# Kernel tuning notes

Measured on AMD Instinct MI355X. Metric: run time of the kernel, lower is better.

Reference implementation:

```python
import jax, jax.numpy as jnp
import numpy as np

# Mamba2 config (from init_kwargs + mamba_ssm Mamba2 defaults)
D_MODEL = 256
D_STATE = 16
D_CONV = 4
EXPAND = 2
HEADDIM = 64                      # Mamba2 default
D_INNER = EXPAND * D_MODEL        # 512
NHEADS = D_INNER // HEADDIM       # 8
CONV_DIM = D_INNER + 2 * D_STATE  # 544 (ngroups=1)
D_IN_PROJ = 2 * D_INNER + 2 * D_STATE + NHEADS  # 1064
B, H, W = 8, 64, 64
EPS = 1e-5


def setup_inputs() -> dict:
    key = jax.random.key(0)
    ks = jax.random.split(key, 8)
    x = jax.random.normal(ks[0], (B, D_MODEL, H, W), jnp.float32)
    ln_w = jnp.ones((D_MODEL,), jnp.float32)
    ln_b = jnp.zeros((D_MODEL,), jnp.float32)
    in_proj_w = jax.random.normal(ks[1], (D_IN_PROJ, D_MODEL), jnp.float32) * (D_MODEL ** -0.5)
    conv_w = jax.random.normal(ks[2], (CONV_DIM, D_CONV), jnp.float32) * (D_CONV ** -0.5)
    conv_b = jnp.zeros((CONV_DIM,), jnp.float32)
    dt = jax.random.uniform(ks[3], (NHEADS,), jnp.float32, 1e-3, 0.1)
    dt_bias = dt + jnp.log(-jnp.expm1(-dt))  # inverse softplus
    A_log = jnp.log(jax.random.uniform(ks[4], (NHEADS,), jnp.float32, 1.0, 16.0))
    D = jnp.ones((NHEADS,), jnp.float32)
    rms_w = jnp.ones((D_INNER,), jnp.float32)
    out_proj_w = jax.random.normal(ks[5], (D_MODEL, D_INNER), jnp.float32) * (D_INNER ** -0.5)
    return dict(x=x, ln_w=ln_w, ln_b=ln_b, in_proj_w=in_proj_w, conv_w=conv_w,
                conv_b=conv_b, dt_bias=dt_bias, A_log=A_log, D=D, rms_w=rms_w,
                out_proj_w=out_proj_w)


def reference(x, ln_w, ln_b, in_proj_w, conv_w, conv_b, dt_bias, A_log, D, rms_w, out_proj_w):
    Bb, C, Hh, Ww = x.shape
    L = Hh * Ww
    # (B,C,H,W) -> (B,L,C)
    xs = x.transpose(0, 2, 3, 1).reshape(Bb, L, C)
    # pre-LayerNorm
    mu = jnp.mean(xs, -1, keepdims=True)
    var = jnp.mean((xs - mu) ** 2, -1, keepdims=True)
    xn = (xs - mu) * jax.lax.rsqrt(var + EPS) * ln_w + ln_b
    # input projection -> z | xBC | dt
    zxbcdt = xn @ in_proj_w.T
    z = zxbcdt[..., :D_INNER]
    xBC = zxbcdt[..., D_INNER:D_INNER + CONV_DIM]
    dt = jax.nn.softplus(zxbcdt[..., D_INNER + CONV_DIM:] + dt_bias)  # (B,L,NH)
    # causal depthwise conv1d (kernel D_CONV) + SiLU
    xp = jnp.pad(xBC, ((0, 0), (D_CONV - 1, 0), (0, 0)))
    conv = conv_b
    for k in range(D_CONV):  # small fixed kernel loop
        conv = conv + xp[:, k:k + L, :] * conv_w[:, k]
    xBC = jax.nn.silu(conv)
    xh = xBC[..., :D_INNER].reshape(Bb, L, NHEADS, HEADDIM)
    Bm = xBC[..., D_INNER:D_INNER + D_STATE]   # (B,L,N)
    Cm = xBC[..., D_INNER + D_STATE:]          # (B,L,N)
    A = -jnp.exp(A_log)                        # (NH,)
    dA = jnp.exp(dt * A)                       # (B,L,NH)
    dtx = dt[..., None] * xh                   # (B,L,NH,P)

    def step(h, inp):
        dA_t, dtx_t, B_t, C_t = inp
        # h: (B,NH,P,N)
        h = dA_t[:, :, None, None] * h + dtx_t[..., None] * B_t[:, None, None, :]
        y = jnp.einsum('bhpn,bn->bhp', h, C_t)
        return h, y

    h0 = jnp.zeros((Bb, NHEADS, HEADDIM, D_STATE), xs.dtype)
    _, ys = jax.lax.scan(step, h0, (dA.transpose(1, 0, 2), dtx.transpose(1, 0, 2, 3),
                                    Bm.transpose(1, 0, 2), Cm.transpose(1, 0, 2)))
    y = ys.transpose(1, 0, 2, 3) + D[:, None] * xh   # (B,L,NH,P)
    y = y.reshape(Bb, L, D_INNER)
    # gated RMSNorm (norm_before_gate=False): rmsnorm(y * silu(z)) * w
    y = y * jax.nn.silu(z)
    y = y * jax.lax.rsqrt(jnp.mean(y * y, -1, keepdims=True) + EPS) * rms_w
    out = y @ out_proj_w.T
    out = out.reshape(Bb, Hh, Ww, C).transpose(0, 3, 1, 2) + x
    return out
```

## Files before the change

kernel.cpp:

```cpp
#include <hip/hip_runtime.h>
#include <cstdint>

typedef unsigned short u16;
typedef unsigned int u32;
typedef u16 u16x8 __attribute__((ext_vector_type(8)));
typedef u16 u16x4 __attribute__((ext_vector_type(4)));
typedef short short8 __attribute__((ext_vector_type(8)));
typedef float f32x4 __attribute__((ext_vector_type(4)));

__device__ __forceinline__ float bf2f(u16 u){ return __uint_as_float(((u32)u)<<16); }
__device__ __forceinline__ u16 f2bf(float f){
  u32 x = __float_as_uint(f);
  return (u16)((x + 0x7fffu + ((x>>16)&1u)) >> 16);
}
__device__ __forceinline__ float siluf(float v){ return v/(1.f + __expf(-v)); }


__global__ __launch_bounds__(256) void k0_wprep(const float* __restrict__ w1,
                                                const float* __restrict__ w2,
                                                u16* __restrict__ w1b, u16* __restrict__ w2b){
  u32 idx = blockIdx.x*256u + threadIdx.x;
  const u32 W1N = 1152u*256u;
  const u32 W2N = 256u*512u;
  if (idx < W1N){
    u32 n = idx >> 8;
    w1b[idx] = (n < 1064u) ? f2bf(w1[idx]) : (u16)0;
  } else if (idx < W1N + W2N){
    u32 j = idx - W1N;
    w2b[j] = f2bf(w2[j]);
  }
}

__global__ __launch_bounds__(256) void k1_ln(const float* __restrict__ x,
                                             const float* __restrict__ ln_w, const float* __restrict__ ln_b,
                                             const float* __restrict__ w1,
                                             u16* __restrict__ xnb, float* __restrict__ dtr){
  __shared__ float tile[256][33];
  __shared__ float mu_s[32], rs_s[32];
  const int b  = blockIdx.y;
  const int l0 = blockIdx.x*32;
  const int tid = threadIdx.x;
  const size_t xbase = (size_t)b*256*4096;
  const int cl = tid>>5;
  const int ll = tid&31;
  for (int cc=0; cc<256; cc+=8){
    int c = cc + cl;
    tile[c][ll] = x[xbase + (size_t)c*4096 + l0 + ll];
  }
  __syncthreads();
  const int lane = tid&63, wave = tid>>6;
  const int lidx = wave*8 + (lane&7);
  const int c0 = (lane>>3)*32;
  float s=0.f, ss=0.f;
  for (int c=c0; c<c0+32; ++c){ float v = tile[c][lidx]; s += v; ss += v*v; }
  for (int off=8; off<64; off<<=1){ s += __shfl_xor(s, off); ss += __shfl_xor(ss, off); }
  float mu = s*(1.f/256.f);
  float var = ss*(1.f/256.f) - mu*mu;
  float rs = rsqrtf(var + 1e-5f);
  if ((lane>>3)==0){ mu_s[lidx]=mu; rs_s[lidx]=rs; }
  __syncthreads();
  {
    const int c = tid;
    const float lw = ln_w[c], lb = ln_b[c];
    for (int l=0; l<32; ++l){
      float v = (tile[c][l]-mu_s[l])*rs_s[l]*lw + lb;
      xnb[((size_t)b*4096 + l0 + l)*256 + c] = f2bf(v);
    }
  }
  {
    const int r = tid>>3, j = tid&7;
    const float* wr = w1 + (size_t)(1056+j)*256;
    const float mur = mu_s[r], rsr = rs_s[r];
    float acc = 0.f;
    for (int c=0; c<256; ++c){
      float v = (tile[c][r]-mur)*rsr*ln_w[c] + ln_b[c];
      acc += v*wr[c];
    }
    dtr[((size_t)b*4096 + l0 + r)*8 + j] = acc;
  }
}

__global__ __launch_bounds__(256) void k2_gemm1(const u16* __restrict__ A, const u16* __restrict__ W,
                                                u16* __restrict__ zb, u16* __restrict__ xbcb){
  __shared__ u16 sA[128*40];
  __shared__ u16 sW[128*40];
  const int tid = threadIdx.x, lane = tid&63, wave = tid>>6;
  const size_t m0 = (size_t)blockIdx.y*128;
  const int n0 = blockIdx.x*128;
  const int wm = (wave>>1)*64, wn = (wave&1)*64;
  f32x4 acc[4][4] = {};
  const int fr = lane&15, kc = (lane>>4)*8;
  for (int k0=0; k0<256; k0+=32){
    #pragma unroll
    for (int j=0; j<2; ++j){
      int ch = j*256 + tid, r = ch>>2, co = (ch&3)*8;
      *(u16x8*)&sA[r*40+co] = *(const u16x8*)&A[(m0+r)*256 + k0 + co];
      *(u16x8*)&sW[r*40+co] = *(const u16x8*)&W[(size_t)(n0+r)*256 + k0 + co];
    }
    __syncthreads();
    short8 af[4], bf4[4];
    #pragma unroll
    for (int fm=0; fm<4; ++fm) af[fm]  = *(short8*)&sA[(wm+fm*16+fr)*40 + kc];
    #pragma unroll
    for (int fn=0; fn<4; ++fn) bf4[fn] = *(short8*)&sW[(wn+fn*16+fr)*40 + kc];
    #pragma unroll
    for (int fm=0; fm<4; ++fm)
      #pragma unroll
      for (int fn=0; fn<4; ++fn)
        acc[fm][fn] = __builtin_amdgcn_mfma_f32_16x16x32_bf16(af[fm],bf4[fn],acc[fm][fn],0,0,0);
    __syncthreads();
  }
  #pragma unroll
  for (int fm=0; fm<4; ++fm)
    #pragma unroll
    for (int fn=0; fn<4; ++fn){
      int rb = wm + fm*16 + ((lane>>4)<<2);
      int col = n0 + wn + fn*16 + (lane&15);
      #pragma unroll
      for (int i=0; i<4; ++i){
        size_t m = m0 + rb + i;
        float v = acc[fm][fn][i];
        if (col < 512)        zb[m*512 + col] = f2bf(v);
        else if (col < 1056)  xbcb[m*544 + (col-512)] = f2bf(v);
      }
    }
}

__global__ __launch_bounds__(256) void kU(const u16* __restrict__ xbcb, const float* __restrict__ dtr,
                                          const float* __restrict__ conv_w, const float* __restrict__ conv_b,
                                          const float* __restrict__ dt_bias, const float* __restrict__ A_log,
                                          float* __restrict__ hend, float* __restrict__ aprod){
  __shared__ char lds[44816];
  float* rawB = (float*)(lds + 0);
  u16*   BcT  = (u16*)(lds + 4560);
  float* wl   = (float*)(lds + 6864);
  const int ck = blockIdx.x, b = blockIdx.y, half = blockIdx.z;
  const int tid = threadIdx.x, lane = tid&63, hh = tid>>6;
  const int h = half*4 + hh;
  const int m0 = b*4096 + ck*64;
  u16* XW = (u16*)(lds + 7888 + hh*9232);
  for (int i=tid; i<67*16; i+=256){
    int r = i>>4, n = i&15; int l = ck*64 - 3 + r;
    rawB[r*17+n] = (l>=0) ? bf2f(xbcb[(size_t)(b*4096+l)*544 + 512 + n]) : 0.f;
  }
  {
    int t = lane;
    float dr = dtr[(size_t)(m0+t)*8 + h] + dt_bias[h];
    float dt = (dr > 20.f) ? dr : log1pf(__expf(dr));
    float Ah = -__expf(A_log[h]);
    float v = dt*Ah;
    #pragma unroll
    for (int off=1; off<64; off<<=1){ float p = __shfl_up(v, off); if (lane >= off) v += p; }
    float scT = __shfl(v, 63);
    wl[hh*64 + t] = dt * __expf(scT - v);
    if (lane==0) aprod[(b*8+h)*64 + ck] = __expf(scT);
  }
  __syncthreads();
  for (int i=tid; i<16*64; i+=256){
    int n = i>>6, s = i&63;
    int c = 512+n;
    float a = conv_b[c] + conv_w[c*4+0]*rawB[s*17+n] + conv_w[c*4+1]*rawB[(s+1)*17+n]
            + conv_w[c*4+2]*rawB[(s+2)*17+n] + conv_w[c*4+3]*rawB[(s+3)*17+n];
    BcT[n*72 + s] = f2bf(siluf(a));
  }
  {
    const int c = h*64 + lane;
    const float w0=conv_w[c*4], w1=conv_w[c*4+1], w2=conv_w[c*4+2], w3=conv_w[c*4+3];
    const float cb = conv_b[c];
    const int lb = ck*64;
    float xm3 = (lb>=3)? bf2f(xbcb[(size_t)(m0-3)*544 + c]) : 0.f;
    float xm2 = (lb>=2)? bf2f(xbcb[(size_t)(m0-2)*544 + c]) : 0.f;
    float xm1 = (lb>=1)? bf2f(xbcb[(size_t)(m0-1)*544 + c]) : 0.f;
    #pragma unroll 4
    for (int t=0; t<64; t+=2){
      float xc0 = bf2f(xbcb[(size_t)(m0+t)*544 + c]);
      float s0v = siluf(cb + w0*xm3 + w1*xm2 + w2*xm1 + w3*xc0) * wl[hh*64 + t];
      xm3=xm2; xm2=xm1; xm1=xc0;
      float xc1 = bf2f(xbcb[(size_t)(m0+t+1)*544 + c]);
      float s1v = siluf(cb + w0*xm3 + w1*xm2 + w2*xm1 + w3*xc1) * wl[hh*64 + t+1];
      xm3=xm2; xm2=xm1; xm1=xc1;
      *(u32*)&XW[lane*72 + t] = (u32)f2bf(s0v) | ((u32)f2bf(s1v)<<16);
    }
  }
  __syncthreads();
  const int fr = lane&15, g = lane>>4;
  f32x4 acc[4] = {};
  #pragma unroll
  for (int ks=0; ks<2; ++ks){
    short8 bfr = *(short8*)&BcT[fr*72 + ks*32 + g*8];
    #pragma unroll
    for (int ti=0; ti<4; ++ti){
      short8 afr = *(short8*)&XW[(ti*16+fr)*72 + ks*32 + g*8];
      acc[ti] = __builtin_amdgcn_mfma_f32_16x16x32_bf16(afr, bfr, acc[ti], 0,0,0);
    }
  }
  size_t hb = ((size_t)((b*8+h)*64 + ck))*64;
  #pragma unroll
  for (int ti=0; ti<4; ++ti)
    #pragma unroll
    for (int i=0; i<4; ++i){
      int p = ti*16 + g*4 + i;
      hend[(hb + p)*16 + fr] = acc[ti][i];
    }
}

__global__ __launch_bounds__(64) void k5_phase2(const float* __restrict__ hend, const float* __restrict__ aprod,
                                                float* __restrict__ hs){
  const int bh = blockIdx.x;
  const int lane = threadIdx.x;
  float hr[16];
  #pragma unroll
  for (int n=0;n<16;++n) hr[n]=0.f;
  for (int ck=0; ck<64; ++ck){
    size_t base = (((size_t)bh*64 + ck)*64 + lane)*16;
    float a = aprod[bh*64 + ck];
    #pragma unroll
    for (int n=0;n<16;++n) hs[base+n] = hr[n];
    #pragma unroll
    for (int n=0;n<16;++n) hr[n] = a*hr[n] + hend[base+n];
  }
}

__global__ __launch_bounds__(256) void kY(const u16* __restrict__ xbcb, const float* __restrict__ dtr,
                                          const float* __restrict__ conv_w, const float* __restrict__ conv_b,
                                          const float* __restrict__ dt_bias, const float* __restrict__ A_log,
                                          const float* __restrict__ Dp, const float* __restrict__ hs,
                                          u16* __restrict__ ybh){
  __shared__ char lds[58560];
  u16*   G     = (u16*)(lds + 0);
  float* rawBC = (float*)(lds + 0);
  u16*   Cc    = (u16*)(lds + 9216);
  u16*   Bc    = (u16*)(lds + 14336);
  float* scs   = (float*)(lds + 19456);
  float* dth   = (float*)(lds + 20544);
  const int ck = blockIdx.x, b = blockIdx.y, half = blockIdx.z;
  const int tid = threadIdx.x, lane = tid&63, hh = tid>>6;
  const int h = half*4 + hh;
  const int m0 = b*4096 + ck*64;
  u16* XT = (u16*)(lds + 21632 + hh*9232);
  for (int i=tid; i<67*32; i+=256){
    int r = i>>5, n = i&31; int l = ck*64 - 3 + r;
    rawBC[r*33+n] = (l>=0) ? bf2f(xbcb[(size_t)(b*4096+l)*544 + 512 + n]) : 0.f;
  }
  {
    int t = lane;
    float dr = dtr[(size_t)(m0+t)*8 + h] + dt_bias[h];
    float dt = (dr > 20.f) ? dr : log1pf(__expf(dr));
    float Ah = -__expf(A_log[h]);
    float v = dt*Ah;
    #pragma unroll
    for (int off=1; off<64; off<<=1){ float p = __shfl_up(v, off); if (lane >= off) v += p; }
    dth[hh*68 + t] = dt;
    scs[hh*68 + t] = v;
  }
  {
    const int c = h*64 + lane;
    const float w0=conv_w[c*4], w1=conv_w[c*4+1], w2=conv_w[c*4+2], w3=conv_w[c*4+3];
    const float cb = conv_b[c];
    const int lb = ck*64;
    float xm3 = (lb>=3)? bf2f(xbcb[(size_t)(m0-3)*544 + c]) : 0.f;
    float xm2 = (lb>=2)? bf2f(xbcb[(size_t)(m0-2)*544 + c]) : 0.f;
    float xm1 = (lb>=1)? bf2f(xbcb[(size_t)(m0-1)*544 + c]) : 0.f;
    #pragma unroll 4
    for (int t=0; t<64; t+=2){
      float xc0 = bf2f(xbcb[(size_t)(m0+t)*544 + c]);
      float s0v = siluf(cb + w0*xm3 + w1*xm2 + w2*xm1 + w3*xc0);
      xm3=xm2; xm2=xm1; xm1=xc0;
      float xc1 = bf2f(xbcb[(size_t)(m0+t+1)*544 + c]);
      float s1v = siluf(cb + w0*xm3 + w1*xm2 + w2*xm1 + w3*xc1);
      xm3=xm2; xm2=xm1; xm1=xc1;
      *(u32*)&XT[lane*72 + t] = (u32)f2bf(s0v) | ((u32)f2bf(s1v)<<16);
    }
  }
  __syncthreads();
  for (int i=tid; i<64*32; i+=256){
    int s = i>>5, n = i&31;
    int c = 512 + n;
    float a = conv_b[c] + conv_w[c*4+0]*rawBC[s*33+n] + conv_w[c*4+1]*rawBC[(s+1)*33+n]
            + conv_w[c*4+2]*rawBC[(s+2)*33+n] + conv_w[c*4+3]*rawBC[(s+3)*33+n];
    u16 v = f2bf(siluf(a));
    if (n < 16) Bc[s*40 + n] = v; else Cc[s*40 + (n-16)] = v;
  }
  for (int i=tid; i<64*16; i+=256){
    int s = i>>4, n = i&15;
    Bc[s*40 + 16 + n] = 0; Cc[s*40 + 16 + n] = 0;
  }
  __syncthreads();
  const int fr = lane&15, g = lane>>4;
  #define GFRAG(TI,SJ) { \
    short8 ca = *(short8*)&Cc[((TI)*16+fr)*40 + g*8]; \
    short8 bb = *(short8*)&Bc[((SJ)*16+fr)*40 + g*8]; \
    f32x4 d = {}; \
    d = __builtin_amdgcn_mfma_f32_16x16x32_bf16(ca, bb, d, 0,0,0); \
    G[((TI)*16 + g*4 + 0)*72 + (SJ)*16 + fr] = f2bf(d[0]); \
    G[((TI)*16 + g*4 + 1)*72 + (SJ)*16 + fr] = f2bf(d[1]); \
    G[((TI)*16 + g*4 + 2)*72 + (SJ)*16 + fr] = f2bf(d[2]); \
    G[((TI)*16 + g*4 + 3)*72 + (SJ)*16 + fr] = f2bf(d[3]); }
  if      (hh==0){ GFRAG(0,0) GFRAG(2,1) GFRAG(3,2) }
  else if (hh==1){ GFRAG(1,0) GFRAG(2,2) GFRAG(3,3) }
  else if (hh==2){ GFRAG(1,1) GFRAG(3,0) }
  else           { GFRAG(2,0) GFRAG(3,1) }
  #undef GFRAG
  __syncthreads();
  f32x4 acc[4][4] = {};
  {
    size_t hsbase = ((size_t)((b*8+h)*64 + ck))*64*16;
    short8 h0f[4];
    #pragma unroll
    for (int pj=0; pj<4; ++pj){
      short8 hf = {0,0,0,0,0,0,0,0};
      if (g < 2){
        int p = pj*16 + fr;
        f32x4 lo = *(const f32x4*)&hs[hsbase + p*16 + g*8];
        f32x4 hi = *(const f32x4*)&hs[hsbase + p*16 + g*8 + 4];
        #pragma unroll
        for (int kk=0; kk<4; ++kk){ hf[kk] = (short)f2bf(lo[kk]); hf[kk+4] = (short)f2bf(hi[kk]); }
      }
      h0f[pj] = hf;
    }
    #pragma unroll
    for (int ti=0; ti<4; ++ti){
      short8 ca = *(short8*)&Cc[(ti*16+fr)*40 + g*8];
      #pragma unroll
      for (int pj=0; pj<4; ++pj)
        acc[ti][pj] = __builtin_amdgcn_mfma_f32_16x16x32_bf16(ca, h0f[pj], acc[ti][pj], 0,0,0);
    }
  }
  #pragma unroll
  for (int ti=0; ti<4; ++ti)
    #pragma unroll
    for (int i=0; i<4; ++i){
      float pt = __expf(scs[hh*68 + ti*16 + g*4 + i]);
      #pragma unroll
      for (int pj=0; pj<4; ++pj) acc[ti][pj][i] *= pt;
    }
  #pragma unroll
  for (int ks=0; ks<2; ++ks){
    short8 xf[4];
    #pragma unroll
    for (int pj=0; pj<4; ++pj) xf[pj] = *(short8*)&XT[(pj*16+fr)*72 + ks*32 + g*8];
    #pragma unroll
    for (int ti=0; ti<4; ++ti){
      if (ks*32 > ti*16+15) continue;
      int t = ti*16 + fr;
      float sct = scs[hh*68 + t];
      f32x4 sc0 = *(f32x4*)&scs[hh*68 + ks*32 + g*8];
      f32x4 sc1 = *(f32x4*)&scs[hh*68 + ks*32 + g*8 + 4];
      f32x4 dt0 = *(f32x4*)&dth[hh*68 + ks*32 + g*8];
      f32x4 dt1 = *(f32x4*)&dth[hh*68 + ks*32 + g*8 + 4];
      u16x8 g8 = *(u16x8*)&G[t*72 + ks*32 + g*8];
      short8 mf;
      #pragma unroll
      for (int kk=0; kk<8; ++kk){
        int s = ks*32 + g*8 + kk;
        float sv = (kk<4) ? sc0[kk] : sc1[kk-4];
        float dv = (kk<4) ? dt0[kk] : dt1[kk-4];
        float m = (s <= t) ? bf2f(g8[kk]) * __expf(sct - sv) * dv : 0.f;
        mf[kk] = (short)f2bf(m);
      }
      #pragma unroll
      for (int pj=0; pj<4; ++pj)
        acc[ti][pj] = __builtin_amdgcn_mfma_f32_16x16x32_bf16(mf, xf[pj], acc[ti][pj], 0,0,0);
    }
  }
  {
    const float Dh = Dp[h];
    #pragma unroll
    for (int ti=0; ti<4; ++ti)
      #pragma unroll
      for (int pj=0; pj<4; ++pj){
        int p = pj*16 + fr;
        u16x4 xv = *(u16x4*)&XT[p*72 + ti*16 + g*4];
        #pragma unroll
        for (int i=0; i<4; ++i) acc[ti][pj][i] += Dh * bf2f(xv[i]);
      }
  }
  #pragma unroll
  for (int ti=0; ti<4; ++ti)
    #pragma unroll
    for (int pj=0; pj<4; ++pj)
      #pragma unroll
      for (int i=0; i<4; ++i)
        XT[(ti*16 + g*4 + i)*72 + pj*16 + fr] = f2bf(acc[ti][pj][i]);
  __syncthreads();
  {
    const int hl = lane>>4;
    const u16* R = (const u16*)(lds + 21632 + hl*9232);
    #pragma unroll
    for (int tt=0; tt<16; ++tt){
      int t = hh*16 + tt;
      u16x4 v = *(const u16x4*)&R[t*72 + (lane&15)*4];
      *(u16x4*)&ybh[(size_t)(m0+t)*512 + half*256 + lane*4] = v;
    }
  }
}

__global__ __launch_bounds__(256) void k7_rms(const u16* __restrict__ y, const u16* __restrict__ zb,
                                              const float* __restrict__ rms_w, u16* __restrict__ ynb){
  const int m = blockIdx.x*4 + (threadIdx.x>>6);
  const int lane = threadIdx.x&63;
  const size_t base = (size_t)m*512 + lane*8;
  u16x8 yv = *(const u16x8*)&y[base];
  u16x8 zv = *(const u16x8*)&zb[base];
  float g[8];
  float ssum = 0.f;
  #pragma unroll
  for (int j=0;j<8;++j){
    float zf = bf2f(zv[j]);
    float sig = 1.f/(1.f + __expf(-zf));
    g[j] = bf2f(yv[j]) * (zf*sig);
    ssum += g[j]*g[j];
  }
  for (int off=1; off<64; off<<=1) ssum += __shfl_xor(ssum, off);
  float rs = rsqrtf(ssum*(1.f/512.f) + 1e-5f);
  u16x8 o;
  #pragma unroll
  for (int j=0;j<8;++j) o[j] = f2bf(g[j]*rs*rms_w[lane*8+j]);
  *(u16x8*)&ynb[base] = o;
}

__global__ __launch_bounds__(256) void k8_gemm2(const u16* __restrict__ A, const u16* __restrict__ W,
                                                const float* __restrict__ xres, float* __restrict__ out){
  __shared__ float smem[4*64*65];
  u16* sA = (u16*)smem;
  u16* sW = ((u16*)smem) + 128*40;
  const int tid = threadIdx.x, lane = tid&63, wave = tid>>6;
  const size_t m0 = (size_t)blockIdx.y*128;
  const int n0 = blockIdx.x*128;
  const int wm = (wave>>1)*64, wn = (wave&1)*64;
  f32x4 acc[4][4] = {};
  const int fr = lane&15, kc = (lane>>4)*8;
  for (int k0=0; k0<512; k0+=32){
    #pragma unroll
    for (int j=0; j<2; ++j){
      int ch = j*256 + tid, r = ch>>2, co = (ch&3)*8;
      *(u16x8*)&sA[r*40+co] = *(const u16x8*)&A[(m0+r)*512 + k0 + co];
      *(u16x8*)&sW[r*40+co] = *(const u16x8*)&W[(size_t)(n0+r)*512 + k0 + co];
    }
    __syncthreads();
    short8 af[4], bf4[4];
    #pragma unroll
    for (int fm=0; fm<4; ++fm) af[fm]  = *(short8*)&sA[(wm+fm*16+fr)*40 + kc];
    #pragma unroll
    for (int fn=0; fn<4; ++fn) bf4[fn] = *(short8*)&sW[(wn+fn*16+fr)*40 + kc];
    #pragma unroll
    for (int fm=0; fm<4; ++fm)
      #pragma unroll
      for (int fn=0; fn<4; ++fn)
        acc[fm][fn] = __builtin_amdgcn_mfma_f32_16x16x32_bf16(af[fm],bf4[fn],acc[fm][fn],0,0,0);
    __syncthreads();
  }
  float* T = smem + wave*(64*65);
  #pragma unroll
  for (int fm=0; fm<4; ++fm)
    #pragma unroll
    for (int fn=0; fn<4; ++fn){
      int rr = fm*16 + ((lane>>4)<<2);
      int cc = fn*16 + (lane&15);
      #pragma unroll
      for (int i=0; i<4; ++i) T[(rr+i)*65 + cc] = acc[fm][fn][i];
    }
  __syncthreads();
  const int bb = (int)(m0>>12);
  const int lbase = (int)(m0&4095) + wm;
  for (int cc=0; cc<64; ++cc){
    int col = n0 + wn + cc;
    size_t o = ((size_t)bb*256 + col)*4096 + lbase + lane;
    out[o] = T[lane*65 + cc] + xres[o];
  }
}

extern "C" void kernel_launch(void* const* d_in, const int* in_sizes, int n_in,
                              void* d_out, int out_size, void* d_ws, size_t ws_size,
                              hipStream_t stream){
  const float* x        = (const float*)d_in[0];
  const float* ln_w     = (const float*)d_in[1];
  const float* ln_b     = (const float*)d_in[2];
  const float* in_proj  = (const float*)d_in[3];
  const float* conv_w   = (const float*)d_in[4];
  const float* conv_b   = (const float*)d_in[5];
  const float* dt_bias  = (const float*)d_in[6];
  const float* A_log    = (const float*)d_in[7];
  const float* Dp       = (const float*)d_in[8];
  const float* rms_w    = (const float*)d_in[9];
  const float* out_proj = (const float*)d_in[10];
  float* out = (float*)d_out;

  char* ws = (char*)d_ws;
  const size_t o_w1   = 0;
  const size_t o_w2   = 589824;
  const size_t o_xn   = 851968;
  const size_t o_z    = 17629184;
  const size_t o_xbcb = 51183616;
  const size_t o_dtr  = 86835200;
  const size_t o_hend = 87883776;
  const size_t o_hs   = 104660992;
  const size_t o_ap   = 121438208;
  const size_t o_ybh  = 121454592;
  const size_t NEED   = 155009024;
  if (ws_size < NEED) return;

  u16*   w1b  = (u16*)(ws + o_w1);
  u16*   w2b  = (u16*)(ws + o_w2);
  u16*   xnb  = (u16*)(ws + o_xn);
  u16*   zbuf = (u16*)(ws + o_z);
  u16*   xbcb = (u16*)(ws + o_xbcb);
  float* dtr  = (float*)(ws + o_dtr);
  float* hend = (float*)(ws + o_hend);
  float* hsb  = (float*)(ws + o_hs);
  float* ap   = (float*)(ws + o_ap);
  u16*   ybh  = (u16*)(ws + o_ybh);
  u16*   ynb  = (u16*)(ws + o_hend);

  k0_wprep<<<1664, 256, 0, stream>>>(in_proj, out_proj, w1b, w2b);
  k1_ln<<<dim3(128, 8), 256, 0, stream>>>(x, ln_w, ln_b, in_proj, xnb, dtr);
  k2_gemm1<<<dim3(9, 256), 256, 0, stream>>>(xnb, w1b, zbuf, xbcb);
  kU<<<dim3(64, 8, 2), 256, 0, stream>>>(xbcb, dtr, conv_w, conv_b, dt_bias, A_log, hend, ap);
  k5_phase2<<<64, 64, 0, stream>>>(hend, ap, hsb);
  kY<<<dim3(64, 8, 2), 256, 0, stream>>>(xbcb, dtr, conv_w, conv_b, dt_bias, A_log, Dp, hsb, ybh);
  k7_rms<<<8192, 256, 0, stream>>>(ybh, zbuf, rms_w, ynb);
  k8_gemm2<<<dim3(2, 256), 256, 0, stream>>>(ynb, w2b, x, out);
}
```

Baseline: 293.4 us.

## Store xBC channel-major from GEMM1 and vectorize conv loads in scan kernels

GEMM1 now writes the conv-input channels transposed, with time contiguous per channel, using 4-wide vector stores. The scan kernels kU and kY read each channel's 64-step window with 16-byte vector loads, replacing strided per-timestep scalar loads with a 544-element row stride. kY also shrinks the B/C LDS tiles from padded 40-wide rows to 16-wide rows and masks the unused K half, and both scan kernels gain a min-blocks launch bound. Both GEMMs get a swizzled 1D block ordering that groups M tiles for L2 reuse. The transposed stores from GEMM1 are strided, which may cost write efficiency.

```diff
diff --git a/kernel.cpp b/kernel.cpp
--- a/kernel.cpp
+++ b/kernel.cpp
@@ -81,12 +81,17 @@
 }
 
 __global__ __launch_bounds__(256) void k2_gemm1(const u16* __restrict__ A, const u16* __restrict__ W,
-                                                u16* __restrict__ zb, u16* __restrict__ xbcb){
+                                                u16* __restrict__ zb, u16* __restrict__ xT){
   __shared__ u16 sA[128*40];
   __shared__ u16 sW[128*40];
   const int tid = threadIdx.x, lane = tid&63, wave = tid>>6;
-  const size_t m0 = (size_t)blockIdx.y*128;
-  const int n0 = blockIdx.x*128;
+  const int s = blockIdx.x;
+  const int kx = s & 7;
+  const int idx = s >> 3;
+  const int xn = idx % 9;
+  const int ym = (idx/9)*8 + kx;
+  const size_t m0 = (size_t)ym*128;
+  const int n0 = xn*128;
   const int wm = (wave>>1)*64, wn = (wave&1)*64;
   f32x4 acc[4][4] = {};
   const int fr = lane&15, kc = (lane>>4)*8;
@@ -116,17 +121,20 @@
     for (int fn=0; fn<4; ++fn){
       int rb = wm + fm*16 + ((lane>>4)<<2);
       int col = n0 + wn + fn*16 + (lane&15);
-      #pragma unroll
-      for (int i=0; i<4; ++i){
-        size_t m = m0 + rb + i;
-        float v = acc[fm][fn][i];
-        if (col < 512)        zb[m*512 + col] = f2bf(v);
-        else if (col < 1056)  xbcb[m*544 + (col-512)] = f2bf(v);
+      size_t m = m0 + rb;
+      if (col < 512){
+        #pragma unroll
+        for (int i=0; i<4; ++i) zb[(m+i)*512 + col] = f2bf(acc[fm][fn][i]);
+      } else if (col < 1056){
+        u16x4 o;
+        #pragma unroll
+        for (int i=0; i<4; ++i) o[i] = f2bf(acc[fm][fn][i]);
+        *(u16x4*)&xT[(size_t)(col-512)*32768 + m] = o;
       }
     }
 }
 
-__global__ __launch_bounds__(256) void kU(const u16* __restrict__ xbcb, const float* __restrict__ dtr,
+__global__ __launch_bounds__(256,3) void kU(const u16* __restrict__ xT, const float* __restrict__ dtr,
                                           const float* __restrict__ conv_w, const float* __restrict__ conv_b,
                                           const float* __restrict__ dt_bias, const float* __restrict__ A_log,
                                           float* __restrict__ hend, float* __restrict__ aprod){
@@ -139,9 +147,12 @@
   const int h = half*4 + hh;
   const int m0 = b*4096 + ck*64;
   u16* XW = (u16*)(lds + 7888 + hh*9232);
-  for (int i=tid; i<67*16; i+=256){
-    int r = i>>4, n = i&15; int l = ck*64 - 3 + r;
-    rawB[r*17+n] = (l>=0) ? bf2f(xbcb[(size_t)(b*4096+l)*544 + 512 + n]) : 0.f;
+  for (int i=tid; i<16*72; i+=256){
+    int n = i/72, r = i - n*72;
+    if (r < 67){
+      int l = ck*64 - 3 + r;
+      rawB[r*17+n] = (l>=0) ? bf2f(xT[(size_t)(512+n)*32768 + (size_t)b*4096 + l]) : 0.f;
+    }
   }
   {
     int t = lane;
@@ -157,41 +168,46 @@
   }
   __syncthreads();
   for (int i=tid; i<16*64; i+=256){
-    int n = i>>6, s = i&63;
+    int n = i>>6, s2 = i&63;
     int c = 512+n;
-    float a = conv_b[c] + conv_w[c*4+0]*rawB[s*17+n] + conv_w[c*4+1]*rawB[(s+1)*17+n]
-            + conv_w[c*4+2]*rawB[(s+2)*17+n] + conv_w[c*4+3]*rawB[(s+3)*17+n];
-    BcT[n*72 + s] = f2bf(siluf(a));
+    float a = conv_b[c] + conv_w[c*4+0]*rawB[s2*17+n] + conv_w[c*4+1]*rawB[(s2+1)*17+n]
+            + conv_w[c*4+2]*rawB[(s2+2)*17+n] + conv_w[c*4+3]*rawB[(s2+3)*17+n];
+    BcT[n*72 + s2] = f2bf(siluf(a));
   }
   {
     const int c = h*64 + lane;
     const float w0=conv_w[c*4], w1=conv_w[c*4+1], w2=conv_w[c*4+2], w3=conv_w[c*4+3];
     const float cb = conv_b[c];
-    const int lb = ck*64;
-    float xm3 = (lb>=3)? bf2f(xbcb[(size_t)(m0-3)*544 + c]) : 0.f;
-    float xm2 = (lb>=2)? bf2f(xbcb[(size_t)(m0-2)*544 + c]) : 0.f;
-    float xm1 = (lb>=1)? bf2f(xbcb[(size_t)(m0-1)*544 + c]) : 0.f;
-    #pragma unroll 4
-    for (int t=0; t<64; t+=2){
-      float xc0 = bf2f(xbcb[(size_t)(m0+t)*544 + c]);
-      float s0v = siluf(cb + w0*xm3 + w1*xm2 + w2*xm1 + w3*xc0) * wl[hh*64 + t];
-      xm3=xm2; xm2=xm1; xm1=xc0;
-      float xc1 = bf2f(xbcb[(size_t)(m0+t+1)*544 + c]);
-      float s1v = siluf(cb + w0*xm3 + w1*xm2 + w2*xm1 + w3*xc1) * wl[hh*64 + t+1];
-      xm3=xm2; xm2=xm1; xm1=xc1;
-      *(u32*)&XW[lane*72 + t] = (u32)f2bf(s0v) | ((u32)f2bf(s1v)<<16);
+    const u16* xcol = xT + (size_t)c*32768 + (size_t)b*4096 + ck*64;
+    u16x8 wv[9]; u16x8 zer = {};
+    wv[0] = (ck>0) ? *(const u16x8*)(xcol - 8) : zer;
+    #pragma unroll
+    for (int j=0;j<8;++j) wv[j+1] = *(const u16x8*)(xcol + j*8);
+    #pragma unroll
+    for (int t8=0; t8<8; ++t8){
+      u16x8 o;
+      #pragma unroll
+      for (int j=0;j<8;++j){
+        const int t = t8*8+j;
+        float x0 = bf2f(wv[(t+5)>>3][(t+5)&7]);
+        float x1 = bf2f(wv[(t+6)>>3][(t+6)&7]);
+        float x2 = bf2f(wv[(t+7)>>3][(t+7)&7]);
+        float x3 = bf2f(wv[(t+8)>>3][(t+8)&7]);
+        o[j] = f2bf(siluf(cb + w0*x0 + w1*x1 + w2*x2 + w3*x3) * wl[hh*64 + t]);
+      }
+      *(u16x8*)&XW[lane*72 + t8*8] = o;
     }
   }
   __syncthreads();
   const int fr = lane&15, g = lane>>4;
-  f32x4 acc[4] = {};
+  f32x4 acc4[4] = {};
   #pragma unroll
   for (int ks=0; ks<2; ++ks){
     short8 bfr = *(short8*)&BcT[fr*72 + ks*32 + g*8];
     #pragma unroll
     for (int ti=0; ti<4; ++ti){
       short8 afr = *(short8*)&XW[(ti*16+fr)*72 + ks*32 + g*8];
-      acc[ti] = __builtin_amdgcn_mfma_f32_16x16x32_bf16(afr, bfr, acc[ti], 0,0,0);
+      acc4[ti] = __builtin_amdgcn_mfma_f32_16x16x32_bf16(afr, bfr, acc4[ti], 0,0,0);
     }
   }
   size_t hb = ((size_t)((b*8+h)*64 + ck))*64;
@@ -200,7 +216,7 @@
     #pragma unroll
     for (int i=0; i<4; ++i){
       int p = ti*16 + g*4 + i;
-      hend[(hb + p)*16 + fr] = acc[ti][i];
+      hend[(hb + p)*16 + fr] = acc4[ti][i];
     }
 }
 
@@ -221,26 +237,29 @@
   }
 }
 
-__global__ __launch_bounds__(256) void kY(const u16* __restrict__ xbcb, const float* __restrict__ dtr,
+__global__ __launch_bounds__(256,3) void kY(const u16* __restrict__ xT, const float* __restrict__ dtr,
                                           const float* __restrict__ conv_w, const float* __restrict__ conv_b,
                                           const float* __restrict__ dt_bias, const float* __restrict__ A_log,
                                           const float* __restrict__ Dp, const float* __restrict__ hs,
                                           u16* __restrict__ ybh){
-  __shared__ char lds[58560];
+  __shared__ char lds[52416];
   u16*   G     = (u16*)(lds + 0);
   float* rawBC = (float*)(lds + 0);
   u16*   Cc    = (u16*)(lds + 9216);
-  u16*   Bc    = (u16*)(lds + 14336);
-  float* scs   = (float*)(lds + 19456);
-  float* dth   = (float*)(lds + 20544);
+  u16*   Bc    = (u16*)(lds + 11264);
+  float* scs   = (float*)(lds + 13312);
+  float* dth   = (float*)(lds + 14400);
   const int ck = blockIdx.x, b = blockIdx.y, half = blockIdx.z;
   const int tid = threadIdx.x, lane = tid&63, hh = tid>>6;
   const int h = half*4 + hh;
   const int m0 = b*4096 + ck*64;
-  u16* XT = (u16*)(lds + 21632 + hh*9232);
-  for (int i=tid; i<67*32; i+=256){
-    int r = i>>5, n = i&31; int l = ck*64 - 3 + r;
-    rawBC[r*33+n] = (l>=0) ? bf2f(xbcb[(size_t)(b*4096+l)*544 + 512 + n]) : 0.f;
+  u16* XT = (u16*)(lds + 15488 + hh*9232);
+  for (int i=tid; i<32*72; i+=256){
+    int n = i/72, r = i - n*72;
+    if (r < 67){
+      int l = ck*64 - 3 + r;
+      rawBC[r*33+n] = (l>=0) ? bf2f(xT[(size_t)(512+n)*32768 + (size_t)b*4096 + l]) : 0.f;
+    }
   }
   {
     int t = lane;
@@ -257,41 +276,42 @@
     const int c = h*64 + lane;
     const float w0=conv_w[c*4], w1=conv_w[c*4+1], w2=conv_w[c*4+2], w3=conv_w[c*4+3];
     const float cb = conv_b[c];
-    const int lb = ck*64;
-    float xm3 = (lb>=3)? bf2f(xbcb[(size_t)(m0-3)*544 + c]) : 0.f;
-    float xm2 = (lb>=2)? bf2f(xbcb[(size_t)(m0-2)*544 + c]) : 0.f;
-    float xm1 = (lb>=1)? bf2f(xbcb[(size_t)(m0-1)*544 + c]) : 0.f;
-    #pragma unroll 4
-    for (int t=0; t<64; t+=2){
-      float xc0 = bf2f(xbcb[(size_t)(m0+t)*544 + c]);
-      float s0v = siluf(cb + w0*xm3 + w1*xm2 + w2*xm1 + w3*xc0);
-      xm3=xm2; xm2=xm1; xm1=xc0;
-      float xc1 = bf2f(xbcb[(size_t)(m0+t+1)*544 + c]);
-      float s1v = siluf(cb + w0*xm3 + w1*xm2 + w2*xm1 + w3*xc1);
-      xm3=xm2; xm2=xm1; xm1=xc1;
-      *(u32*)&XT[lane*72 + t] = (u32)f2bf(s0v) | ((u32)f2bf(s1v)<<16);
+    const u16* xcol = xT + (size_t)c*32768 + (size_t)b*4096 + ck*64;
+    u16x8 wv[9]; u16x8 zer = {};
+    wv[0] = (ck>0) ? *(const u16x8*)(xcol - 8) : zer;
+    #pragma unroll
+    for (int j=0;j<8;++j) wv[j+1] = *(const u16x8*)(xcol + j*8);
+    #pragma unroll
+    for (int t8=0; t8<8; ++t8){
+      u16x8 o;
+      #pragma unroll
+      for (int j=0;j<8;++j){
+        const int t = t8*8+j;
+        float x0 = bf2f(wv[(t+5)>>3][(t+5)&7]);
+        float x1 = bf2f(wv[(t+6)>>3][(t+6)&7]);
+        float x2 = bf2f(wv[(t+7)>>3][(t+7)&7]);
+        float x3 = bf2f(wv[(t+8)>>3][(t+8)&7]);
+        o[j] = f2bf(siluf(cb + w0*x0 + w1*x1 + w2*x2 + w3*x3));
+      }
+      *(u16x8*)&XT[lane*72 + t8*8] = o;
     }
   }
   __syncthreads();
   for (int i=tid; i<64*32; i+=256){
-    int s = i>>5, n = i&31;
+    int s2 = i>>5, n = i&31;
     int c = 512 + n;
-    float a = conv_b[c] + conv_w[c*4+0]*rawBC[s*33+n] + conv_w[c*4+1]*rawBC[(s+1)*33+n]
-            + conv_w[c*4+2]*rawBC[(s+2)*33+n] + conv_w[c*4+3]*rawBC[(s+3)*33+n];
+    float a = conv_b[c] + conv_w[c*4+0]*rawBC[s2*33+n] + conv_w[c*4+1]*rawBC[(s2+1)*33+n]
+            + conv_w[c*4+2]*rawBC[(s2+2)*33+n] + conv_w[c*4+3]*rawBC[(s2+3)*33+n];
     u16 v = f2bf(siluf(a));
-    if (n < 16) Bc[s*40 + n] = v; else Cc[s*40 + (n-16)] = v;
-  }
-  for (int i=tid; i<64*16; i+=256){
-    int s = i>>4, n = i&15;
-    Bc[s*40 + 16 + n] = 0; Cc[s*40 + 16 + n] = 0;
+    if (n < 16) Bc[s2*16 + n] = v; else Cc[s2*16 + (n-16)] = v;
   }
   __syncthreads();
   const int fr = lane&15, g = lane>>4;
   #define GFRAG(TI,SJ) { \
-    short8 ca = *(short8*)&Cc[((TI)*16+fr)*40 + g*8]; \
-    short8 bb = *(short8*)&Bc[((SJ)*16+fr)*40 + g*8]; \
+    short8 ca = {}, bb = {}; \
+    if (g < 2){ ca = *(short8*)&Cc[((TI)*16+fr)*16 + g*8]; bb = *(short8*)&Bc[((SJ)*16+fr)*16 + g*8]; } \
     f32x4 d = {}; \
-    d = __builtin_amdgcn_mfma_f32_16x16x32_bf16(ca, bb, d, 0,0,0); \
+    d = __builtin_amdgcn_mfma_f32_16x16x32_bf16(ca,bb,d,0,0,0); \
     G[((TI)*16 + g*4 + 0)*72 + (SJ)*16 + fr] = f2bf(d[0]); \
     G[((TI)*16 + g*4 + 1)*72 + (SJ)*16 + fr] = f2bf(d[1]); \
     G[((TI)*16 + g*4 + 2)*72 + (SJ)*16 + fr] = f2bf(d[2]); \
@@ -308,7 +328,7 @@
     short8 h0f[4];
     #pragma unroll
     for (int pj=0; pj<4; ++pj){
-      short8 hf = {0,0,0,0,0,0,0,0};
+      short8 hf = {};
       if (g < 2){
         int p = pj*16 + fr;
         f32x4 lo = *(const f32x4*)&hs[hsbase + p*16 + g*8];
@@ -320,7 +340,8 @@
     }
     #pragma unroll
     for (int ti=0; ti<4; ++ti){
-      short8 ca = *(short8*)&Cc[(ti*16+fr)*40 + g*8];
+      short8 ca = {};
+      if (g < 2) ca = *(short8*)&Cc[(ti*16+fr)*16 + g*8];
       #pragma unroll
       for (int pj=0; pj<4; ++pj)
         acc[ti][pj] = __builtin_amdgcn_mfma_f32_16x16x32_bf16(ca, h0f[pj], acc[ti][pj], 0,0,0);
@@ -352,10 +373,10 @@
       short8 mf;
       #pragma unroll
       for (int kk=0; kk<8; ++kk){
-        int s = ks*32 + g*8 + kk;
+        int s2 = ks*32 + g*8 + kk;
         float sv = (kk<4) ? sc0[kk] : sc1[kk-4];
         float dv = (kk<4) ? dt0[kk] : dt1[kk-4];
-        float m = (s <= t) ? bf2f(g8[kk]) * __expf(sct - sv) * dv : 0.f;
+        float m = (s2 <= t) ? bf2f(g8[kk]) * __expf(sct - sv) * dv : 0.f;
         mf[kk] = (short)f2bf(m);
       }
       #pragma unroll
@@ -385,7 +406,7 @@
   __syncthreads();
   {
     const int hl = lane>>4;
-    const u16* R = (const u16*)(lds + 21632 + hl*9232);
+    const u16* R = (const u16*)(lds + 15488 + hl*9232);
     #pragma unroll
     for (int tt=0; tt<16; ++tt){
       int t = hh*16 + tt;
@@ -425,8 +446,13 @@
   u16* sA = (u16*)smem;
   u16* sW = ((u16*)smem) + 128*40;
   const int tid = threadIdx.x, lane = tid&63, wave = tid>>6;
-  const size_t m0 = (size_t)blockIdx.y*128;
-  const int n0 = blockIdx.x*128;
+  const int s = blockIdx.x;
+  const int kx = s & 7;
+  const int idx = s >> 3;
+  const int xn = idx & 1;
+  const int ym = (idx>>1)*8 + kx;
+  const size_t m0 = (size_t)ym*128;
+  const int n0 = xn*128;
   const int wm = (wave>>1)*64, wn = (wave&1)*64;
   f32x4 acc[4][4] = {};
   const int fr = lane&15, kc = (lane>>4)*8;
@@ -491,7 +517,7 @@
   const size_t o_w2   = 589824;
   const size_t o_xn   = 851968;
   const size_t o_z    = 17629184;
-  const size_t o_xbcb = 51183616;
+  const size_t o_xT   = 51183616;
   const size_t o_dtr  = 86835200;
   const size_t o_hend = 87883776;
   const size_t o_hs   = 104660992;
@@ -504,7 +530,7 @@
   u16*   w2b  = (u16*)(ws + o_w2);
   u16*   xnb  = (u16*)(ws + o_xn);
   u16*   zbuf = (u16*)(ws + o_z);
-  u16*   xbcb = (u16*)(ws + o_xbcb);
+  u16*   xTb  = (u16*)(ws + o_xT);
   float* dtr  = (float*)(ws + o_dtr);
   float* hend = (float*)(ws + o_hend);
   float* hsb  = (float*)(ws + o_hs);
@@ -514,10 +540,10 @@
 
   k0_wprep<<<1664, 256, 0, stream>>>(in_proj, out_proj, w1b, w2b);
   k1_ln<<<dim3(128, 8), 256, 0, stream>>>(x, ln_w, ln_b, in_proj, xnb, dtr);
-  k2_gemm1<<<dim3(9, 256), 256, 0, stream>>>(xnb, w1b, zbuf, xbcb);
-  kU<<<dim3(64, 8, 2), 256, 0, stream>>>(xbcb, dtr, conv_w, conv_b, dt_bias, A_log, hend, ap);
+  k2_gemm1<<<2304, 256, 0, stream>>>(xnb, w1b, zbuf, xTb);
+  kU<<<dim3(64, 8, 2), 256, 0, stream>>>(xTb, dtr, conv_w, conv_b, dt_bias, A_log, hend, ap);
   k5_phase2<<<64, 64, 0, stream>>>(hend, ap, hsb);
-  kY<<<dim3(64, 8, 2), 256, 0, stream>>>(xbcb, dtr, conv_w, conv_b, dt_bias, A_log, Dp, hsb, ybh);
+  kY<<<dim3(64, 8, 2), 256, 0, stream>>>(xTb, dtr, conv_w, conv_b, dt_bias, A_log, Dp, hsb, ybh);
   k7_rms<<<8192, 256, 0, stream>>>(ybh, zbuf, rms_w, ynb);
-  k8_gemm2<<<dim3(2, 256), 256, 0, stream>>>(ynb, w2b, x, out);
-}
+  k8_gemm2<<<512, 256, 0, stream>>>(ynb, w2b, x, out);
+}
```

After: 284.9 us. -2.9%, faster.
